# Optimization experiments

Hardware: AMD Instinct MI355X
Metric: run time of the kernel (lower is better)

## Reference

```python
import jax, jax.numpy as jnp
import numpy as np

N_BINS = 500
TAIL = 1.0
MIN_W = 1e-3
MIN_H = 1e-3
MIN_D = 1e-3
WIN_A = -10000.0
WIN_B = 10000.0

N_CELLS = 128
N_GENES_OI = 300
N_GENES = 1000
N_LATENT = 64
N_HID = 32
N_FRAG = 50000
N_CELLS_TOTAL = 5000
N_SPLINE = 3 * N_BINS - 1  # 1499


def _bn(x, g, b, eps=1e-5):
    # torch BatchNorm1d in training mode: batch stats, biased variance
    m = x.mean(0)
    v = x.var(0)
    return (x - m) / jnp.sqrt(v + eps) * g + b


def _rqs_inverse_logdet(y, uw, uh, ud):
    """Unconstrained rational-quadratic spline, inverse pass; returns logdet [F].
    y: [F]; uw, uh: [F, N_BINS]; ud: [F, N_BINS-1]."""
    nb = uw.shape[-1]
    const = float(np.log(np.exp(1.0 - MIN_D) - 1.0))
    ud = jnp.pad(ud, ((0, 0), (1, 1)), constant_values=const)  # [F, nb+1] linear tails
    inside = (y >= -TAIL) & (y <= TAIL)
    yc = jnp.clip(y, -TAIL, TAIL)

    w = jax.nn.softmax(uw, axis=-1)
    w = MIN_W + (1.0 - MIN_W * nb) * w
    cw = jnp.pad(jnp.cumsum(w, axis=-1), ((0, 0), (1, 0)))
    cw = 2.0 * TAIL * cw - TAIL
    cw = cw.at[:, 0].set(-TAIL).at[:, -1].set(TAIL)
    w = cw[:, 1:] - cw[:, :-1]

    h = jax.nn.softmax(uh, axis=-1)
    h = MIN_H + (1.0 - MIN_H * nb) * h
    ch = jnp.pad(jnp.cumsum(h, axis=-1), ((0, 0), (1, 0)))
    ch = 2.0 * TAIL * ch - TAIL
    ch = ch.at[:, 0].set(-TAIL).at[:, -1].set(TAIL)
    h = ch[:, 1:] - ch[:, :-1]

    d = MIN_D + jax.nn.softplus(ud)  # [F, nb+1]

    # inverse: bucketize y against cumheights
    idx = jnp.clip(jnp.sum(yc[:, None] >= ch, axis=-1) - 1, 0, nb - 1)  # [F]
    take = lambda t, i: jnp.take_along_axis(t, i[:, None], axis=-1)[:, 0]
    cw_k = take(cw, idx)
    w_k = take(w, idx)
    ch_k = take(ch, idx)
    h_k = take(h, idx)
    d_k = take(d, idx)
    d_k1 = take(d, idx + 1)

    delta = h_k / w_k
    s = d_k + d_k1 - 2.0 * delta
    dy = yc - ch_k
    qa = dy * s + h_k * (delta - d_k)
    qb = h_k * d_k - dy * s
    qc = -delta * dy
    disc = qb * qb - 4.0 * qa * qc
    root = (2.0 * qc) / (-qb - jnp.sqrt(disc))  # theta in [0,1]
    th1m = root * (1.0 - root)
    den = delta + s * th1m
    num = (delta * delta) * (d_k1 * root * root + 2.0 * delta * th1m + d_k * (1.0 - root) * (1.0 - root))
    logabsdet = jnp.log(num) - 2.0 * jnp.log(den)
    return jnp.where(inside, -logabsdet, 0.0)


def setup_inputs() -> dict:
    key = jax.random.key(0)
    ks = jax.random.split(key, 16)
    ab = WIN_B - WIN_A
    latent = jax.random.normal(ks[0], (N_CELLS, N_LATENT), jnp.float32)
    coordinates = WIN_A + ab * jax.random.uniform(ks[1], (N_FRAG, 2), jnp.float32)
    W1 = jax.random.normal(ks[2], (N_LATENT, N_HID), jnp.float32) / np.sqrt(N_LATENT)
    b1 = jax.random.normal(ks[3], (N_HID,), jnp.float32) * 0.01
    g1 = jnp.ones((N_HID,), jnp.float32)
    be1 = jnp.zeros((N_HID,), jnp.float32)
    W2 = jax.random.normal(ks[4], (N_HID, N_HID), jnp.float32) / np.sqrt(N_HID)
    b2 = jax.random.normal(ks[5], (N_HID,), jnp.float32) * 0.01
    g2 = jnp.ones((N_HID,), jnp.float32)
    be2 = jnp.zeros((N_HID,), jnp.float32)
    stdv = 1.0 / np.sqrt(N_HID) / 100.0
    spline_w = jax.random.uniform(ks[6], (N_GENES, N_HID, N_SPLINE), jnp.float32, -stdv, stdv)
    rho_w = jax.random.uniform(ks[7], (N_GENES, N_HID), jnp.float32, -1.0 / 100.0, 1.0 / 100.0)
    default_init = float(np.log(np.exp(1.0 - MIN_D) - 1.0))
    mix_spline = default_init + 0.1 * jax.random.normal(ks[8], (N_GENES, N_SPLINE), jnp.float32)
    rho_bias = 1e-4 + 1e-3 * jax.random.uniform(ks[9], (N_GENES,), jnp.float32)
    libsize = 500.0 + 4500.0 * jax.random.uniform(ks[10], (N_CELLS_TOTAL,), jnp.float32)
    genes_oi = jax.random.randint(ks[11], (N_GENES_OI,), 0, N_GENES, jnp.int32)
    cells_oi = jax.random.randint(ks[12], (N_CELLS,), 0, N_CELLS_TOTAL, jnp.int32)
    local_cellxgene_ix = jax.random.randint(ks[13], (N_FRAG,), 0, N_CELLS * N_GENES_OI, jnp.int32)
    local_gene_ix = local_cellxgene_ix % N_GENES_OI
    return {
        "latent": latent, "coordinates": coordinates,
        "W1": W1, "b1": b1, "g1": g1, "be1": be1,
        "W2": W2, "b2": b2, "g2": g2, "be2": be2,
        "spline_w": spline_w, "rho_w": rho_w, "mix_spline": mix_spline,
        "rho_bias": rho_bias, "libsize": libsize,
        "genes_oi": genes_oi, "cells_oi": cells_oi,
        "local_cellxgene_ix": local_cellxgene_ix, "local_gene_ix": local_gene_ix,
    }


def reference(latent, coordinates, W1, b1, g1, be1, W2, b2, g2, be2,
              spline_w, rho_w, mix_spline, rho_bias, libsize,
              genes_oi, cells_oi, local_cellxgene_ix, local_gene_ix):
    ab = WIN_B - WIN_A
    # decoder MLP (Linear -> ReLU -> BatchNorm, x2)
    h = _bn(jax.nn.relu(latent @ W1 + b1), g1, be1)
    h = _bn(jax.nn.relu(h @ W2 + b2), g2, be2)  # [C, H]
    sw = spline_w[genes_oi]                      # [G, H, D]
    spline = jnp.einsum('ch,ghd->cgd', h, sw)    # [C, G, D]
    rho = h @ rho_w[genes_oi].T                  # [C, G]
    C, G, D = spline.shape
    spline_frag = spline.reshape(C * G, D)[local_cellxgene_ix]   # [F, D]
    params = mix_spline[genes_oi][local_gene_ix] + spline_frag   # [F, D]
    uw = params[:, :N_BINS]
    uh = params[:, N_BINS:2 * N_BINS]
    ud = params[:, 2 * N_BINS:]

    def logp(val):  # val: [F]
        x = ((val - WIN_A) / ab - 0.5) * 2.0
        return jnp.log(0.5) + _rqs_inverse_logdet(x, uw, uh, ud) - jnp.log(ab)

    ll_loci = logp(coordinates[:, 0]).sum() + logp(coordinates[:, 1]).sum()

    rate = rho_bias[genes_oi] * jnp.exp(rho) * libsize[cells_oi][:, None]  # [C, G]
    counts = jnp.zeros(C * G, jnp.float32).at[local_cellxgene_ix].add(1.0).reshape(C, G)
    ll_counts = counts * jnp.log(rate) - rate - jax.lax.lgamma(counts + 1.0)

    elbo = -(ll_loci + ll_counts.sum())
    return elbo
```

## Files before the change

### kernel.cpp

```cpp
#include <hip/hip_runtime.h>
#include <math.h>

#define N_BINSK  500
#define N_SPL    1499
#define N_CELLSK 128
#define N_GOI    300
#define N_HIDK   32
#define N_LATK   64
#define N_FRAGK  50000
#define N_PAIR   (N_CELLSK * N_GOI)
#define WIN_A_F  (-10000.0f)
#define AB_F     (20000.0f)

#define CELLS_PB 8
#define N_TILES  (N_CELLSK / CELLS_PB)
#define CSTRIDE  1012
#define DPADF    1504
#define NCHUNK   24
#define CAP      16

#define WS_HIST   0
#define WS_ACC    (N_PAIR * 4)
#define WS_H      (WS_ACC + 128 * 8)
#define WS_BUCKET (WS_H + N_CELLSK * N_HIDK * 4)
#define WS_HBF    (WS_BUCKET + N_PAIR * CAP * 2)
#define WS_SWGT   (WS_HBF + N_CELLSK * N_HIDK * 2)
#define WS_ZERO   (WS_H)

#define PREP_BLOCKS (N_GOI * NCHUNK)
#define HIST_BLOCKS 196
#define GENE_GRID   (304 * N_TILES)

typedef __attribute__((ext_vector_type(8))) short bf16x8;
typedef __attribute__((ext_vector_type(4))) float f32x4;

__device__ __forceinline__ unsigned short f2bf(float f)
{
    union { float f; unsigned u; } c; c.f = f;
    return (unsigned short)((c.u + 0x7FFF + ((c.u >> 16) & 1)) >> 16);
}
__device__ __forceinline__ float bf2f(short b)
{
    union { unsigned u; float f; } c;
    c.u = ((unsigned)(unsigned short)b) << 16;
    return c.f;
}
__device__ __forceinline__ float frcp(float x) { return __builtin_amdgcn_rcpf(x); }

__global__ __launch_bounds__(256) void prep_mlp_bucket_kernel(
    const float* __restrict__ spline_w, const int* __restrict__ genes_oi,
    unsigned short* __restrict__ swgt,
    const float* __restrict__ latent, const float* __restrict__ W1, const float* __restrict__ b1,
    const float* __restrict__ g1, const float* __restrict__ be1,
    const float* __restrict__ W2, const float* __restrict__ b2,
    const float* __restrict__ g2, const float* __restrict__ be2,
    float* __restrict__ h_out, unsigned short* __restrict__ h_bf,
    const int* __restrict__ lcx, int* __restrict__ hist,
    unsigned short* __restrict__ bucket)
{
    __shared__ float Ls[N_HIDK][65];
    const int bid = blockIdx.x;
    const int t = threadIdx.x;

    if (bid < PREP_BLOCKS) {
        const int gl = bid / NCHUNK;
        const int chunk = bid - gl * NCHUNK;
        const int g = genes_oi[gl];
        const int dl = t & 63, h0 = t >> 6;
        const int dbase = chunk * 64;

        const float* src = spline_w + (size_t)g * (N_HIDK * N_SPL);
        #pragma unroll
        for (int p = 0; p < 8; ++p) {
            const int hid = h0 + p * 4;
            Ls[hid][dl] = (dbase + dl < N_SPL) ? src[(size_t)hid * N_SPL + dbase + dl] : 0.f;
        }
        __syncthreads();

        const int dim = dbase + (t >> 2);
        if (dim < DPADF) {
            const int hseg = (t & 3) * 8;
            unsigned short out[8];
            #pragma unroll
            for (int j = 0; j < 8; ++j) out[j] = f2bf(Ls[hseg + j][t >> 2]);
            *(uint4*)(swgt + ((size_t)(gl * DPADF + dim) * N_HIDK + hseg)) = *(const uint4*)out;
        }
        return;
    }
    if (bid < PREP_BLOCKS + HIST_BLOCKS) {
        const int f = (bid - PREP_BLOCKS) * 256 + t;
        if (f < N_FRAGK) {
            const int p = lcx[f];
            const int slot = atomicAdd(&hist[p], 1);
            if (slot < CAP) bucket[(size_t)p * CAP + slot] = (unsigned short)f;
        }
        return;
    }

    __shared__ float A[N_CELLSK][N_HIDK + 1];
    __shared__ float mean_s[N_HIDK], rstd_s[N_HIDK];
    const int c = t;
    const bool act = (c < N_CELLSK);

    float x[N_LATK];
    if (act) {
        #pragma unroll
        for (int i = 0; i < N_LATK; ++i) x[i] = latent[c * N_LATK + i];
        for (int j = 0; j < N_HIDK; ++j) {
            float a = b1[j];
            #pragma unroll
            for (int i = 0; i < N_LATK; ++i) a = fmaf(x[i], W1[i * N_HIDK + j], a);
            A[c][j] = fmaxf(a, 0.0f);
        }
    }
    __syncthreads();
    if (c < N_HIDK) {
        float m = 0.f;
        for (int i = 0; i < N_CELLSK; ++i) m += A[i][c];
        m *= (1.0f / N_CELLSK);
        float v = 0.f;
        for (int i = 0; i < N_CELLSK; ++i) { float d = A[i][c] - m; v += d * d; }
        v *= (1.0f / N_CELLSK);
        mean_s[c] = m;
        rstd_s[c] = rsqrtf(v + 1e-5f);
    }
    __syncthreads();
    float hb[N_HIDK];
    if (act) {
        #pragma unroll
        for (int j = 0; j < N_HIDK; ++j)
            hb[j] = (A[c][j] - mean_s[j]) * rstd_s[j] * g1[j] + be1[j];
    }
    __syncthreads();
    if (act) {
        for (int j = 0; j < N_HIDK; ++j) {
            float a = b2[j];
            #pragma unroll
            for (int i = 0; i < N_HIDK; ++i) a = fmaf(hb[i], W2[i * N_HIDK + j], a);
            A[c][j] = fmaxf(a, 0.0f);
        }
    }
    __syncthreads();
    if (c < N_HIDK) {
        float m = 0.f;
        for (int i = 0; i < N_CELLSK; ++i) m += A[i][c];
        m *= (1.0f / N_CELLSK);
        float v = 0.f;
        for (int i = 0; i < N_CELLSK; ++i) { float d = A[i][c] - m; v += d * d; }
        v *= (1.0f / N_CELLSK);
        mean_s[c] = m;
        rstd_s[c] = rsqrtf(v + 1e-5f);
    }
    __syncthreads();
    if (act) {
        #pragma unroll
        for (int j = 0; j < N_HIDK; ++j) {
            const float v = (A[c][j] - mean_s[j]) * rstd_s[j] * g2[j] + be2[j];
            h_out[c * N_HIDK + j] = v;
            h_bf[c * N_HIDK + j] = f2bf(v);
        }
    }
}

__global__ __launch_bounds__(512, 8) void gene_kernel(
    const float* __restrict__ h, const unsigned short* __restrict__ h_bf,
    const unsigned short* __restrict__ swgt,
    const float* __restrict__ mix_spline,
    const int* __restrict__ genes_oi, const float* __restrict__ coords,
    const int* __restrict__ hist, const unsigned short* __restrict__ bucket,
    const float* __restrict__ rho_w, const float* __restrict__ rho_bias,
    const float* __restrict__ libsize, const int* __restrict__ cells_oi,
    double* __restrict__ acc)
{
    __shared__ float P[CELLS_PB * CSTRIDE];
    __shared__ float hL[CELLS_PB][36];
    __shared__ int al_s[CELLS_PB];
    __shared__ int acnt_s[CELLS_PB + 1];
    __shared__ int wcnt[2];

    const int bid = blockIdx.x;
    const int t = threadIdx.x;
    const int lane = t & 63;
    const int w = t >> 6;

    if (bid >= GENE_GRID) {
        const int pgl = bid - GENE_GRID;
        const int g = genes_oi[pgl];
        float v = 0.f;
        if (t < N_CELLSK) {
            const int cnt = hist[t * N_GOI + pgl];
            const float* hrow = h + t * N_HIDK;
            const float* rwp = rho_w + g * N_HIDK;
            float rho = 0.f;
            #pragma unroll
            for (int i = 0; i < N_HIDK; ++i) rho = fmaf(hrow[i], rwp[i], rho);
            const float rate = rho_bias[g] * __expf(rho) * libsize[cells_oi[t]];
            const float cf = (float)cnt;
            v = cf * __logf(rate) - rate - lgammaf(cf + 1.0f);
        }
        #pragma unroll
        for (int o = 32; o; o >>= 1) v += __shfl_xor(v, o);
        if (lane == 0 && w < 2) atomicAdd(&acc[pgl & 127], (double)v);
        return;
    }

    const int r  = bid & 7;
    const int m_ = bid >> 3;
    const int ct = m_ & 15;
    const int gl = (m_ >> 4) * 8 + r;
    if (gl >= N_GOI) return;

    const int cellcnt = (t < N_CELLSK) ? hist[t * N_GOI + gl] : 0;
    const unsigned long long mk = __ballot(cellcnt > 0);
    if (lane == 0 && w < 2) wcnt[w] = (int)__popcll(mk);
    __syncthreads();
    const int nag = wcnt[0] + wcnt[1];
    if (cellcnt > 0) {
        const int pos = ((w == 1) ? wcnt[0] : 0)
                      + (int)__popcll(mk & ((1ull << lane) - 1ull)) - ct * CELLS_PB;
        if (pos >= 0 && pos < CELLS_PB) { al_s[pos] = t; acnt_s[pos] = min(cellcnt, CAP); }
    }
    __syncthreads();
    if (ct * CELLS_PB >= nag) return;
    const int nv = min(CELLS_PB, nag - ct * CELLS_PB);

    if (t == 0) {
        int run = 0;
        #pragma unroll
        for (int s = 0; s < CELLS_PB; ++s) {
            const int c = (s < nv) ? acnt_s[s] : 0;
            acnt_s[s] = run; run += c;
        }
        acnt_s[CELLS_PB] = run;
    }
    if (t < nv * N_HIDK) {
        const int s = t >> 5, i = t & 31;
        hL[s][i] = h[al_s[s] * N_HIDK + i];
    }

    const int g  = genes_oi[gl];
    const float* mixg = mix_spline + (size_t)g * N_SPL;

    {
        const int koff = (lane >> 4) * 8;
        const int acell = al_s[min(lane & 7, nv - 1)];
        const bf16x8 afrag = *(const bf16x8*)(h_bf + acell * N_HIDK + koff);
        const int dcol = lane & 15;
        #pragma unroll 1
        for (int tile = w; tile < 63; tile += 8) {
            const int d = tile * 16 + dcol;
            const bf16x8 bfrag = *(const bf16x8*)(swgt + ((size_t)(gl * DPADF + d) * N_HIDK + koff));
            const float m = mixg[min(d, 999)];
            f32x4 acc4 = {m, m, m, m};
            acc4 = __builtin_amdgcn_mfma_f32_16x16x32_bf16(afrag, bfrag, acc4, 0, 0, 0);
            if (lane < 32 && d < 1000) {
                const int s = d + ((d >= N_BINSK) ? 4 : 0);
                #pragma unroll
                for (int rr = 0; rr < 4; ++rr)
                    P[((lane >> 4) * 4 + rr) * CSTRIDE + s] = __expf(acc4[rr]);
            }
        }
    }
    __syncthreads();

    for (int s = w; s < 2 * nv; s += 8) {
        float* Pb = P + (s >> 1) * CSTRIDE + ((s & 1) ? 504 : 0);
        const int base = lane * 8;
        float v[8], pre[8];
        if (lane < 62) {
            *(float4*)&v[0] = *(const float4*)&Pb[base];
            *(float4*)&v[4] = *(const float4*)&Pb[base + 4];
        } else if (lane == 62) {
            *(float4*)&v[0] = *(const float4*)&Pb[base];
            v[4] = v[5] = v[6] = v[7] = 0.f;
        } else {
            #pragma unroll
            for (int k = 0; k < 8; ++k) v[k] = 0.f;
        }
        float run = 0.f;
        #pragma unroll
        for (int k = 0; k < 8; ++k) { pre[k] = run; run += v[k]; }
        float sv = run;
        #pragma unroll
        for (int o = 1; o < 64; o <<= 1) {
            float tt = __shfl_up(sv, o);
            if (lane >= o) sv += tt;
        }
        const float tot = __shfl(sv, 63);
        const float invT = frcp(tot);
        const float excl = sv - run;
        #pragma unroll
        for (int k = 0; k < 8; ++k)
            pre[k] = fmaf((float)(base + k), 0.002f, -1.0f) + (excl + pre[k]) * invT;
        if (lane < 63) {
            *(float4*)&Pb[base]     = *(const float4*)&pre[0];
            *(float4*)&Pb[base + 4] = *(const float4*)&pre[4];
        }
    }
    __syncthreads();

    float contrib = 0.f;
    const int ncb = acnt_s[CELLS_PB] * 2;
    if (t < ncb) {
        const int fi = t >> 1;
        int s = 0;
        #pragma unroll
        for (int k = 1; k < CELLS_PB; ++k) s += (acnt_s[k] <= fi) ? 1 : 0;
        const int cell = al_s[s];
        const int fid = bucket[(size_t)(cell * N_GOI + gl) * CAP + (fi - acnt_s[s])];
        const float val = coords[fid * 2 + (t & 1)];
        const float yc = ((val - WIN_A_F) / AB_F - 0.5f) * 2.0f;
        if (yc >= -1.0f && yc <= 1.0f) {
            const float* CWc = P + s * CSTRIDE;
            const float* CHc = CWc + 504;

            int j = (int)fminf(fmaxf((yc + 1.0f) * 250.0f, 0.0f), 499.0f);
            if (CHc[j] <= yc) {
                while (j < 500 && CHc[j + 1] <= yc) ++j;
            } else {
                do { --j; } while (CHc[j] > yc);
            }
            const int idx = min(j, N_BINSK - 1);

            const int bcol = 999 + min(max(idx, 1), 498);
            const unsigned short* rud = swgt + (size_t)(gl * DPADF + bcol) * N_HIDK;
            float dA = 0.f, dB = 0.f;
            #pragma unroll
            for (int c8 = 0; c8 < 4; ++c8) {
                const bf16x8 va = *(const bf16x8*)(rud + c8 * 8);
                const bf16x8 vb = *(const bf16x8*)(rud + N_HIDK + c8 * 8);
                const float4 h0 = *(const float4*)&hL[s][c8 * 8];
                const float4 h1 = *(const float4*)&hL[s][c8 * 8 + 4];
                dA = fmaf(h0.x, bf2f(va[0]), dA); dB = fmaf(h0.x, bf2f(vb[0]), dB);
                dA = fmaf(h0.y, bf2f(va[1]), dA); dB = fmaf(h0.y, bf2f(vb[1]), dB);
                dA = fmaf(h0.z, bf2f(va[2]), dA); dB = fmaf(h0.z, bf2f(vb[2]), dB);
                dA = fmaf(h0.w, bf2f(va[3]), dA); dB = fmaf(h0.w, bf2f(vb[3]), dB);
                dA = fmaf(h1.x, bf2f(va[4]), dA); dB = fmaf(h1.x, bf2f(vb[4]), dB);
                dA = fmaf(h1.y, bf2f(va[5]), dA); dB = fmaf(h1.y, bf2f(vb[5]), dB);
                dA = fmaf(h1.z, bf2f(va[6]), dA); dB = fmaf(h1.z, bf2f(vb[6]), dB);
                dA = fmaf(h1.w, bf2f(va[7]), dA); dB = fmaf(h1.w, bf2f(vb[7]), dB);
            }
            float udA = 0.f, udB = 0.f;
            if (idx == 0)                 udB = dA + mixg[1000];
            else if (idx == N_BINSK - 1)  udA = dB + mixg[1498];
            else { udA = dA + mixg[bcol]; udB = dB + mixg[bcol + 1]; }
            const float d_k  = (idx == 0)           ? 1.0f
                             : 0.001f + __logf(1.0f + __expf(udA));
            const float d_k1 = (idx == N_BINSK - 1) ? 1.0f
                             : 0.001f + __logf(1.0f + __expf(udB));

            const float ch_k  = CHc[idx];
            const float h_k   = CHc[idx + 1] - ch_k;
            const float w_k   = CWc[idx + 1] - CWc[idx];

            const float delta = h_k * frcp(w_k);
            const float s2 = d_k + d_k1 - 2.0f * delta;
            const float dy = yc - ch_k;
            const float qa = dy * s2 + h_k * (delta - d_k);
            const float qb = h_k * d_k - dy * s2;
            const float qc = -delta * dy;
            const float disc = qb * qb - 4.0f * qa * qc;
            const float root = 2.0f * qc * frcp(-qb - sqrtf(disc));
            const float th1m = root * (1.0f - root);
            const float den = delta + s2 * th1m;
            const float num = delta * delta *
                (d_k1 * root * root + 2.0f * delta * th1m + d_k * (1.0f - root) * (1.0f - root));
            const float rd = frcp(den);
            contrib -= __logf(num * rd * rd);
        }
    }
    #pragma unroll
    for (int o = 32; o; o >>= 1) contrib += __shfl_xor(contrib, o);
    if (lane == 0 && contrib != 0.0f)
        atomicAdd(&acc[(bid ^ (w << 3)) & 127], (double)contrib);
}

__global__ __launch_bounds__(64) void final_kernel(const double* __restrict__ acc,
                                                   float* __restrict__ out)
{
    const int lane = threadIdx.x;
    double s = acc[lane] + acc[lane + 64];
    #pragma unroll
    for (int o = 32; o; o >>= 1) s += __shfl_down(s, o);
    if (lane == 0) {
        const double c0 = (double)(2 * N_FRAGK) * (log(0.5) - log((double)AB_F));
        out[0] = (float)(-(s + c0));
    }
}

extern "C" void kernel_launch(void* const* d_in, const int* in_sizes, int n_in,
                              void* d_out, int out_size, void* d_ws, size_t ws_size,
                              hipStream_t stream)
{
    const float* latent   = (const float*)d_in[0];
    const float* coords   = (const float*)d_in[1];
    const float* W1       = (const float*)d_in[2];
    const float* b1       = (const float*)d_in[3];
    const float* g1       = (const float*)d_in[4];
    const float* be1      = (const float*)d_in[5];
    const float* W2       = (const float*)d_in[6];
    const float* b2       = (const float*)d_in[7];
    const float* g2       = (const float*)d_in[8];
    const float* be2      = (const float*)d_in[9];
    const float* spline_w = (const float*)d_in[10];
    const float* rho_w    = (const float*)d_in[11];
    const float* mix      = (const float*)d_in[12];
    const float* rho_bias = (const float*)d_in[13];
    const float* libsize  = (const float*)d_in[14];
    const int* genes_oi   = (const int*)d_in[15];
    const int* cells_oi   = (const int*)d_in[16];
    const int* lcx        = (const int*)d_in[17];

    char* ws = (char*)d_ws;
    int*            hist   = (int*)(ws + WS_HIST);
    double*         acc    = (double*)(ws + WS_ACC);
    float*          h_ws   = (float*)(ws + WS_H);
    unsigned short* bucket = (unsigned short*)(ws + WS_BUCKET);
    unsigned short* h_bf   = (unsigned short*)(ws + WS_HBF);
    unsigned short* swgt   = (unsigned short*)(ws + WS_SWGT);

    hipMemsetAsync(d_ws, 0, WS_ZERO, stream);

    hipLaunchKernelGGL(prep_mlp_bucket_kernel, dim3(PREP_BLOCKS + HIST_BLOCKS + 1), dim3(256), 0, stream,
                       spline_w, genes_oi, swgt,
                       latent, W1, b1, g1, be1, W2, b2, g2, be2, h_ws, h_bf, lcx, hist, bucket);
    hipLaunchKernelGGL(gene_kernel, dim3(GENE_GRID + N_GOI), dim3(512), 0, stream,
                       h_ws, h_bf, swgt, mix, genes_oi, coords,
                       hist, bucket, rho_w, rho_bias, libsize, cells_oi, acc);
    hipLaunchKernelGGL(final_kernel, dim3(1), dim3(64), 0, stream, acc, (float*)d_out);
}
```

Baseline: 110.0 us.

## Fold final reduction into gene kernel via last-block counter; reorder prep blocks

Removes the separate final_kernel launch: each gene_kernel block increments a done counter after its atomic accumulation, and the last block sums the accumulators and writes the output. The prep kernel is also reordered so the serial MLP block and the histogram blocks are scheduled first, ahead of the many spline-weight conversion blocks, so the long-running MLP block is not left as a tail. This adds a global atomic and memory fences per block in exchange for one fewer kernel launch.

```diff
diff --git a/kernel.cpp b/kernel.cpp
--- a/kernel.cpp
+++ b/kernel.cpp
@@ -21,7 +21,8 @@
 
 #define WS_HIST   0
 #define WS_ACC    (N_PAIR * 4)
-#define WS_H      (WS_ACC + 128 * 8)
+#define WS_CNT    (WS_ACC + 128 * 8)
+#define WS_H      (WS_CNT + 16)
 #define WS_BUCKET (WS_H + N_CELLSK * N_HIDK * 4)
 #define WS_HBF    (WS_BUCKET + N_PAIR * CAP * 2)
 #define WS_SWGT   (WS_HBF + N_CELLSK * N_HIDK * 2)
@@ -30,6 +31,7 @@
 #define PREP_BLOCKS (N_GOI * NCHUNK)
 #define HIST_BLOCKS 196
 #define GENE_GRID   (304 * N_TILES)
+#define GENE_TOTAL  (GENE_GRID + N_GOI)
 
 typedef __attribute__((ext_vector_type(8))) short bf16x8;
 typedef __attribute__((ext_vector_type(4))) float f32x4;
@@ -62,33 +64,74 @@
     const int bid = blockIdx.x;
     const int t = threadIdx.x;
 
-    if (bid < PREP_BLOCKS) {
-        const int gl = bid / NCHUNK;
-        const int chunk = bid - gl * NCHUNK;
-        const int g = genes_oi[gl];
-        const int dl = t & 63, h0 = t >> 6;
-        const int dbase = chunk * 64;
-
-        const float* src = spline_w + (size_t)g * (N_HIDK * N_SPL);
-        #pragma unroll
-        for (int p = 0; p < 8; ++p) {
-            const int hid = h0 + p * 4;
-            Ls[hid][dl] = (dbase + dl < N_SPL) ? src[(size_t)hid * N_SPL + dbase + dl] : 0.f;
-        }
-        __syncthreads();
-
-        const int dim = dbase + (t >> 2);
-        if (dim < DPADF) {
-            const int hseg = (t & 3) * 8;
-            unsigned short out[8];
-            #pragma unroll
-            for (int j = 0; j < 8; ++j) out[j] = f2bf(Ls[hseg + j][t >> 2]);
-            *(uint4*)(swgt + ((size_t)(gl * DPADF + dim) * N_HIDK + hseg)) = *(const uint4*)out;
+    if (bid == 0) {
+        __shared__ float A[N_CELLSK][N_HIDK + 1];
+        __shared__ float mean_s[N_HIDK], rstd_s[N_HIDK];
+        const int c = t;
+        const bool act = (c < N_CELLSK);
+
+        float x[N_LATK];
+        if (act) {
+            #pragma unroll
+            for (int i = 0; i < N_LATK; ++i) x[i] = latent[c * N_LATK + i];
+            for (int j = 0; j < N_HIDK; ++j) {
+                float a = b1[j];
+                #pragma unroll
+                for (int i = 0; i < N_LATK; ++i) a = fmaf(x[i], W1[i * N_HIDK + j], a);
+                A[c][j] = fmaxf(a, 0.0f);
+            }
+        }
+        __syncthreads();
+        if (c < N_HIDK) {
+            float m = 0.f;
+            for (int i = 0; i < N_CELLSK; ++i) m += A[i][c];
+            m *= (1.0f / N_CELLSK);
+            float v = 0.f;
+            for (int i = 0; i < N_CELLSK; ++i) { float d = A[i][c] - m; v += d * d; }
+            v *= (1.0f / N_CELLSK);
+            mean_s[c] = m;
+            rstd_s[c] = rsqrtf(v + 1e-5f);
+        }
+        __syncthreads();
+        float hb[N_HIDK];
+        if (act) {
+            #pragma unroll
+            for (int j = 0; j < N_HIDK; ++j)
+                hb[j] = (A[c][j] - mean_s[j]) * rstd_s[j] * g1[j] + be1[j];
+        }
+        __syncthreads();
+        if (act) {
+            for (int j = 0; j < N_HIDK; ++j) {
+                float a = b2[j];
+                #pragma unroll
+                for (int i = 0; i < N_HIDK; ++i) a = fmaf(hb[i], W2[i * N_HIDK + j], a);
+                A[c][j] = fmaxf(a, 0.0f);
+            }
+        }
+        __syncthreads();
+        if (c < N_HIDK) {
+            float m = 0.f;
+            for (int i = 0; i < N_CELLSK; ++i) m += A[i][c];
+            m *= (1.0f / N_CELLSK);
+            float v = 0.f;
+            for (int i = 0; i < N_CELLSK; ++i) { float d = A[i][c] - m; v += d * d; }
+            v *= (1.0f / N_CELLSK);
+            mean_s[c] = m;
+            rstd_s[c] = rsqrtf(v + 1e-5f);
+        }
+        __syncthreads();
+        if (act) {
+            #pragma unroll
+            for (int j = 0; j < N_HIDK; ++j) {
+                const float v = (A[c][j] - mean_s[j]) * rstd_s[j] * g2[j] + be2[j];
+                h_out[c * N_HIDK + j] = v;
+                h_bf[c * N_HIDK + j] = f2bf(v);
+            }
         }
         return;
     }
-    if (bid < PREP_BLOCKS + HIST_BLOCKS) {
-        const int f = (bid - PREP_BLOCKS) * 256 + t;
+    if (bid <= HIST_BLOCKS) {
+        const int f = (bid - 1) * 256 + t;
         if (f < N_FRAGK) {
             const int p = lcx[f];
             const int slot = atomicAdd(&hist[p], 1);
@@ -97,68 +140,28 @@
         return;
     }
 
-    __shared__ float A[N_CELLSK][N_HIDK + 1];
-    __shared__ float mean_s[N_HIDK], rstd_s[N_HIDK];
-    const int c = t;
-    const bool act = (c < N_CELLSK);
-
-    float x[N_LATK];
-    if (act) {
+    const int pb = bid - HIST_BLOCKS - 1;
+    const int gl = pb / NCHUNK;
+    const int chunk = pb - gl * NCHUNK;
+    const int g = genes_oi[gl];
+    const int dl = t & 63, h0 = t >> 6;
+    const int dbase = chunk * 64;
+
+    const float* src = spline_w + (size_t)g * (N_HIDK * N_SPL);
+    #pragma unroll
+    for (int p = 0; p < 8; ++p) {
+        const int hid = h0 + p * 4;
+        Ls[hid][dl] = (dbase + dl < N_SPL) ? src[(size_t)hid * N_SPL + dbase + dl] : 0.f;
+    }
+    __syncthreads();
+
+    const int dim = dbase + (t >> 2);
+    if (dim < DPADF) {
+        const int hseg = (t & 3) * 8;
+        unsigned short out[8];
         #pragma unroll
-        for (int i = 0; i < N_LATK; ++i) x[i] = latent[c * N_LATK + i];
-        for (int j = 0; j < N_HIDK; ++j) {
-            float a = b1[j];
-            #pragma unroll
-            for (int i = 0; i < N_LATK; ++i) a = fmaf(x[i], W1[i * N_HIDK + j], a);
-            A[c][j] = fmaxf(a, 0.0f);
-        }
-    }
-    __syncthreads();
-    if (c < N_HIDK) {
-        float m = 0.f;
-        for (int i = 0; i < N_CELLSK; ++i) m += A[i][c];
-        m *= (1.0f / N_CELLSK);
-        float v = 0.f;
-        for (int i = 0; i < N_CELLSK; ++i) { float d = A[i][c] - m; v += d * d; }
-        v *= (1.0f / N_CELLSK);
-        mean_s[c] = m;
-        rstd_s[c] = rsqrtf(v + 1e-5f);
-    }
-    __syncthreads();
-    float hb[N_HIDK];
-    if (act) {
-        #pragma unroll
-        for (int j = 0; j < N_HIDK; ++j)
-            hb[j] = (A[c][j] - mean_s[j]) * rstd_s[j] * g1[j] + be1[j];
-    }
-    __syncthreads();
-    if (act) {
-        for (int j = 0; j < N_HIDK; ++j) {
-            float a = b2[j];
-            #pragma unroll
-            for (int i = 0; i < N_HIDK; ++i) a = fmaf(hb[i], W2[i * N_HIDK + j], a);
-            A[c][j] = fmaxf(a, 0.0f);
-        }
-    }
-    __syncthreads();
-    if (c < N_HIDK) {
-        float m = 0.f;
-        for (int i = 0; i < N_CELLSK; ++i) m += A[i][c];
-        m *= (1.0f / N_CELLSK);
-        float v = 0.f;
-        for (int i = 0; i < N_CELLSK; ++i) { float d = A[i][c] - m; v += d * d; }
-        v *= (1.0f / N_CELLSK);
-        mean_s[c] = m;
-        rstd_s[c] = rsqrtf(v + 1e-5f);
-    }
-    __syncthreads();
-    if (act) {
-        #pragma unroll
-        for (int j = 0; j < N_HIDK; ++j) {
-            const float v = (A[c][j] - mean_s[j]) * rstd_s[j] * g2[j] + be2[j];
-            h_out[c * N_HIDK + j] = v;
-            h_bf[c * N_HIDK + j] = f2bf(v);
-        }
+        for (int j = 0; j < 8; ++j) out[j] = f2bf(Ls[hseg + j][t >> 2]);
+        *(uint4*)(swgt + ((size_t)(gl * DPADF + dim) * N_HIDK + hseg)) = *(const uint4*)out;
     }
 }
 
@@ -170,221 +173,228 @@
     const int* __restrict__ hist, const unsigned short* __restrict__ bucket,
     const float* __restrict__ rho_w, const float* __restrict__ rho_bias,
     const float* __restrict__ libsize, const int* __restrict__ cells_oi,
-    double* __restrict__ acc)
+    double* __restrict__ acc, int* __restrict__ cnt_done, float* __restrict__ out)
 {
     __shared__ float P[CELLS_PB * CSTRIDE];
     __shared__ float hL[CELLS_PB][36];
     __shared__ int al_s[CELLS_PB];
     __shared__ int acnt_s[CELLS_PB + 1];
     __shared__ int wcnt[2];
+    __shared__ int lastFlag;
 
     const int bid = blockIdx.x;
     const int t = threadIdx.x;
     const int lane = t & 63;
     const int w = t >> 6;
 
-    if (bid >= GENE_GRID) {
-        const int pgl = bid - GENE_GRID;
-        const int g = genes_oi[pgl];
-        float v = 0.f;
-        if (t < N_CELLSK) {
-            const int cnt = hist[t * N_GOI + pgl];
-            const float* hrow = h + t * N_HIDK;
-            const float* rwp = rho_w + g * N_HIDK;
-            float rho = 0.f;
-            #pragma unroll
-            for (int i = 0; i < N_HIDK; ++i) rho = fmaf(hrow[i], rwp[i], rho);
-            const float rate = rho_bias[g] * __expf(rho) * libsize[cells_oi[t]];
-            const float cf = (float)cnt;
-            v = cf * __logf(rate) - rate - lgammaf(cf + 1.0f);
+    do {
+        if (bid >= GENE_GRID) {
+            const int pgl = bid - GENE_GRID;
+            const int g = genes_oi[pgl];
+            float v = 0.f;
+            if (t < N_CELLSK) {
+                const int cnt = hist[t * N_GOI + pgl];
+                const float* hrow = h + t * N_HIDK;
+                const float* rwp = rho_w + g * N_HIDK;
+                float rho = 0.f;
+                #pragma unroll
+                for (int i = 0; i < N_HIDK; ++i) rho = fmaf(hrow[i], rwp[i], rho);
+                const float rate = rho_bias[g] * __expf(rho) * libsize[cells_oi[t]];
+                const float cf = (float)cnt;
+                v = cf * __logf(rate) - rate - lgammaf(cf + 1.0f);
+            }
+            #pragma unroll
+            for (int o = 32; o; o >>= 1) v += __shfl_xor(v, o);
+            if (lane == 0 && w < 2) atomicAdd(&acc[pgl & 127], (double)v);
+            break;
+        }
+
+        const int r  = bid & 7;
+        const int m_ = bid >> 3;
+        const int ct = m_ & 15;
+        const int gl = (m_ >> 4) * 8 + r;
+        if (gl >= N_GOI) break;
+
+        const int cellcnt = (t < N_CELLSK) ? hist[t * N_GOI + gl] : 0;
+        const unsigned long long mk = __ballot(cellcnt > 0);
+        if (lane == 0 && w < 2) wcnt[w] = (int)__popcll(mk);
+        __syncthreads();
+        const int nag = wcnt[0] + wcnt[1];
+        if (cellcnt > 0) {
+            const int pos = ((w == 1) ? wcnt[0] : 0)
+                          + (int)__popcll(mk & ((1ull << lane) - 1ull)) - ct * CELLS_PB;
+            if (pos >= 0 && pos < CELLS_PB) { al_s[pos] = t; acnt_s[pos] = min(cellcnt, CAP); }
+        }
+        __syncthreads();
+        if (ct * CELLS_PB >= nag) break;
+        const int nv = min(CELLS_PB, nag - ct * CELLS_PB);
+
+        if (t == 0) {
+            int run = 0;
+            #pragma unroll
+            for (int s = 0; s < CELLS_PB; ++s) {
+                const int c = (s < nv) ? acnt_s[s] : 0;
+                acnt_s[s] = run; run += c;
+            }
+            acnt_s[CELLS_PB] = run;
+        }
+        if (t < nv * N_HIDK) {
+            const int s = t >> 5, i = t & 31;
+            hL[s][i] = h[al_s[s] * N_HIDK + i];
+        }
+
+        const int g  = genes_oi[gl];
+        const float* mixg = mix_spline + (size_t)g * N_SPL;
+
+        {
+            const int koff = (lane >> 4) * 8;
+            const int acell = al_s[min(lane & 7, nv - 1)];
+            const bf16x8 afrag = *(const bf16x8*)(h_bf + acell * N_HIDK + koff);
+            const int dcol = lane & 15;
+            #pragma unroll 1
+            for (int tile = w; tile < 63; tile += 8) {
+                const int d = tile * 16 + dcol;
+                const bf16x8 bfrag = *(const bf16x8*)(swgt + ((size_t)(gl * DPADF + d) * N_HIDK + koff));
+                const float m = mixg[min(d, 999)];
+                f32x4 acc4 = {m, m, m, m};
+                acc4 = __builtin_amdgcn_mfma_f32_16x16x32_bf16(afrag, bfrag, acc4, 0, 0, 0);
+                if (lane < 32 && d < 1000) {
+                    const int s = d + ((d >= N_BINSK) ? 4 : 0);
+                    #pragma unroll
+                    for (int rr = 0; rr < 4; ++rr)
+                        P[((lane >> 4) * 4 + rr) * CSTRIDE + s] = __expf(acc4[rr]);
+                }
+            }
+        }
+        __syncthreads();
+
+        for (int s = w; s < 2 * nv; s += 8) {
+            float* Pb = P + (s >> 1) * CSTRIDE + ((s & 1) ? 504 : 0);
+            const int base = lane * 8;
+            float v[8], pre[8];
+            if (lane < 62) {
+                *(float4*)&v[0] = *(const float4*)&Pb[base];
+                *(float4*)&v[4] = *(const float4*)&Pb[base + 4];
+            } else if (lane == 62) {
+                *(float4*)&v[0] = *(const float4*)&Pb[base];
+                v[4] = v[5] = v[6] = v[7] = 0.f;
+            } else {
+                #pragma unroll
+                for (int k = 0; k < 8; ++k) v[k] = 0.f;
+            }
+            float run = 0.f;
+            #pragma unroll
+            for (int k = 0; k < 8; ++k) { pre[k] = run; run += v[k]; }
+            float sv = run;
+            #pragma unroll
+            for (int o = 1; o < 64; o <<= 1) {
+                float tt = __shfl_up(sv, o);
+                if (lane >= o) sv += tt;
+            }
+            const float tot = __shfl(sv, 63);
+            const float invT = frcp(tot);
+            const float excl = sv - run;
+            #pragma unroll
+            for (int k = 0; k < 8; ++k)
+                pre[k] = fmaf((float)(base + k), 0.002f, -1.0f) + (excl + pre[k]) * invT;
+            if (lane < 63) {
+                *(float4*)&Pb[base]     = *(const float4*)&pre[0];
+                *(float4*)&Pb[base + 4] = *(const float4*)&pre[4];
+            }
+        }
+        __syncthreads();
+
+        float contrib = 0.f;
+        const int ncb = acnt_s[CELLS_PB] * 2;
+        if (t < ncb) {
+            const int fi = t >> 1;
+            int s = 0;
+            #pragma unroll
+            for (int k = 1; k < CELLS_PB; ++k) s += (acnt_s[k] <= fi) ? 1 : 0;
+            const int cell = al_s[s];
+            const int fid = bucket[(size_t)(cell * N_GOI + gl) * CAP + (fi - acnt_s[s])];
+            const float val = coords[fid * 2 + (t & 1)];
+            const float yc = ((val - WIN_A_F) / AB_F - 0.5f) * 2.0f;
+            if (yc >= -1.0f && yc <= 1.0f) {
+                const float* CWc = P + s * CSTRIDE;
+                const float* CHc = CWc + 504;
+
+                int j = (int)fminf(fmaxf((yc + 1.0f) * 250.0f, 0.0f), 499.0f);
+                if (CHc[j] <= yc) {
+                    while (j < 500 && CHc[j + 1] <= yc) ++j;
+                } else {
+                    do { --j; } while (CHc[j] > yc);
+                }
+                const int idx = min(j, N_BINSK - 1);
+
+                const int bcol = 999 + min(max(idx, 1), 498);
+                const unsigned short* rud = swgt + (size_t)(gl * DPADF + bcol) * N_HIDK;
+                float dA = 0.f, dB = 0.f;
+                #pragma unroll
+                for (int c8 = 0; c8 < 4; ++c8) {
+                    const bf16x8 va = *(const bf16x8*)(rud + c8 * 8);
+                    const bf16x8 vb = *(const bf16x8*)(rud + N_HIDK + c8 * 8);
+                    const float4 h0 = *(const float4*)&hL[s][c8 * 8];
+                    const float4 h1 = *(const float4*)&hL[s][c8 * 8 + 4];
+                    dA = fmaf(h0.x, bf2f(va[0]), dA); dB = fmaf(h0.x, bf2f(vb[0]), dB);
+                    dA = fmaf(h0.y, bf2f(va[1]), dA); dB = fmaf(h0.y, bf2f(vb[1]), dB);
+                    dA = fmaf(h0.z, bf2f(va[2]), dA); dB = fmaf(h0.z, bf2f(vb[2]), dB);
+                    dA = fmaf(h0.w, bf2f(va[3]), dA); dB = fmaf(h0.w, bf2f(vb[3]), dB);
+                    dA = fmaf(h1.x, bf2f(va[4]), dA); dB = fmaf(h1.x, bf2f(vb[4]), dB);
+                    dA = fmaf(h1.y, bf2f(va[5]), dA); dB = fmaf(h1.y, bf2f(vb[5]), dB);
+                    dA = fmaf(h1.z, bf2f(va[6]), dA); dB = fmaf(h1.z, bf2f(vb[6]), dB);
+                    dA = fmaf(h1.w, bf2f(va[7]), dA); dB = fmaf(h1.w, bf2f(vb[7]), dB);
+                }
+                float udA = 0.f, udB = 0.f;
+                if (idx == 0)                 udB = dA + mixg[1000];
+                else if (idx == N_BINSK - 1)  udA = dB + mixg[1498];
+                else { udA = dA + mixg[bcol]; udB = dB + mixg[bcol + 1]; }
+                const float d_k  = (idx == 0)           ? 1.0f
+                                 : 0.001f + __logf(1.0f + __expf(udA));
+                const float d_k1 = (idx == N_BINSK - 1) ? 1.0f
+                                 : 0.001f + __logf(1.0f + __expf(udB));
+
+                const float ch_k  = CHc[idx];
+                const float h_k   = CHc[idx + 1] - ch_k;
+                const float w_k   = CWc[idx + 1] - CWc[idx];
+
+                const float delta = h_k * frcp(w_k);
+                const float s2 = d_k + d_k1 - 2.0f * delta;
+                const float dy = yc - ch_k;
+                const float qa = dy * s2 + h_k * (delta - d_k);
+                const float qb = h_k * d_k - dy * s2;
+                const float qc = -delta * dy;
+                const float disc = qb * qb - 4.0f * qa * qc;
+                const float root = 2.0f * qc * frcp(-qb - sqrtf(disc));
+                const float th1m = root * (1.0f - root);
+                const float den = delta + s2 * th1m;
+                const float num = delta * delta *
+                    (d_k1 * root * root + 2.0f * delta * th1m + d_k * (1.0f - root) * (1.0f - root));
+                const float rd = frcp(den);
+                contrib -= __logf(num * rd * rd);
+            }
         }
         #pragma unroll
-        for (int o = 32; o; o >>= 1) v += __shfl_xor(v, o);
-        if (lane == 0 && w < 2) atomicAdd(&acc[pgl & 127], (double)v);
-        return;
-    }
-
-    const int r  = bid & 7;
-    const int m_ = bid >> 3;
-    const int ct = m_ & 15;
-    const int gl = (m_ >> 4) * 8 + r;
-    if (gl >= N_GOI) return;
-
-    const int cellcnt = (t < N_CELLSK) ? hist[t * N_GOI + gl] : 0;
-    const unsigned long long mk = __ballot(cellcnt > 0);
-    if (lane == 0 && w < 2) wcnt[w] = (int)__popcll(mk);
+        for (int o = 32; o; o >>= 1) contrib += __shfl_xor(contrib, o);
+        if (lane == 0 && contrib != 0.0f)
+            atomicAdd(&acc[(bid ^ (w << 3)) & 127], (double)contrib);
+    } while (0);
+
     __syncthreads();
-    const int nag = wcnt[0] + wcnt[1];
-    if (cellcnt > 0) {
-        const int pos = ((w == 1) ? wcnt[0] : 0)
-                      + (int)__popcll(mk & ((1ull << lane) - 1ull)) - ct * CELLS_PB;
-        if (pos >= 0 && pos < CELLS_PB) { al_s[pos] = t; acnt_s[pos] = min(cellcnt, CAP); }
+    if (t == 0) {
+        __threadfence();
+        lastFlag = (atomicAdd(cnt_done, 1) == GENE_TOTAL - 1) ? 1 : 0;
     }
     __syncthreads();
-    if (ct * CELLS_PB >= nag) return;
-    const int nv = min(CELLS_PB, nag - ct * CELLS_PB);
-
-    if (t == 0) {
-        int run = 0;
+    if (lastFlag && t < 64) {
+        __threadfence();
+        double s = acc[t] + acc[t + 64];
         #pragma unroll
-        for (int s = 0; s < CELLS_PB; ++s) {
-            const int c = (s < nv) ? acnt_s[s] : 0;
-            acnt_s[s] = run; run += c;
-        }
-        acnt_s[CELLS_PB] = run;
-    }
-    if (t < nv * N_HIDK) {
-        const int s = t >> 5, i = t & 31;
-        hL[s][i] = h[al_s[s] * N_HIDK + i];
-    }
-
-    const int g  = genes_oi[gl];
-    const float* mixg = mix_spline + (size_t)g * N_SPL;
-
-    {
-        const int koff = (lane >> 4) * 8;
-        const int acell = al_s[min(lane & 7, nv - 1)];
-        const bf16x8 afrag = *(const bf16x8*)(h_bf + acell * N_HIDK + koff);
-        const int dcol = lane & 15;
-        #pragma unroll 1
-        for (int tile = w; tile < 63; tile += 8) {
-            const int d = tile * 16 + dcol;
-            const bf16x8 bfrag = *(const bf16x8*)(swgt + ((size_t)(gl * DPADF + d) * N_HIDK + koff));
-            const float m = mixg[min(d, 999)];
-            f32x4 acc4 = {m, m, m, m};
-            acc4 = __builtin_amdgcn_mfma_f32_16x16x32_bf16(afrag, bfrag, acc4, 0, 0, 0);
-            if (lane < 32 && d < 1000) {
-                const int s = d + ((d >= N_BINSK) ? 4 : 0);
-                #pragma unroll
-                for (int rr = 0; rr < 4; ++rr)
-                    P[((lane >> 4) * 4 + rr) * CSTRIDE + s] = __expf(acc4[rr]);
-            }
-        }
-    }
-    __syncthreads();
-
-    for (int s = w; s < 2 * nv; s += 8) {
-        float* Pb = P + (s >> 1) * CSTRIDE + ((s & 1) ? 504 : 0);
-        const int base = lane * 8;
-        float v[8], pre[8];
-        if (lane < 62) {
-            *(float4*)&v[0] = *(const float4*)&Pb[base];
-            *(float4*)&v[4] = *(const float4*)&Pb[base + 4];
-        } else if (lane == 62) {
-            *(float4*)&v[0] = *(const float4*)&Pb[base];
-            v[4] = v[5] = v[6] = v[7] = 0.f;
-        } else {
-            #pragma unroll
-            for (int k = 0; k < 8; ++k) v[k] = 0.f;
-        }
-        float run = 0.f;
-        #pragma unroll
-        for (int k = 0; k < 8; ++k) { pre[k] = run; run += v[k]; }
-        float sv = run;
-        #pragma unroll
-        for (int o = 1; o < 64; o <<= 1) {
-            float tt = __shfl_up(sv, o);
-            if (lane >= o) sv += tt;
-        }
-        const float tot = __shfl(sv, 63);
-        const float invT = frcp(tot);
-        const float excl = sv - run;
-        #pragma unroll
-        for (int k = 0; k < 8; ++k)
-            pre[k] = fmaf((float)(base + k), 0.002f, -1.0f) + (excl + pre[k]) * invT;
-        if (lane < 63) {
-            *(float4*)&Pb[base]     = *(const float4*)&pre[0];
-            *(float4*)&Pb[base + 4] = *(const float4*)&pre[4];
-        }
-    }
-    __syncthreads();
-
-    float contrib = 0.f;
-    const int ncb = acnt_s[CELLS_PB] * 2;
-    if (t < ncb) {
-        const int fi = t >> 1;
-        int s = 0;
-        #pragma unroll
-        for (int k = 1; k < CELLS_PB; ++k) s += (acnt_s[k] <= fi) ? 1 : 0;
-        const int cell = al_s[s];
-        const int fid = bucket[(size_t)(cell * N_GOI + gl) * CAP + (fi - acnt_s[s])];
-        const float val = coords[fid * 2 + (t & 1)];
-        const float yc = ((val - WIN_A_F) / AB_F - 0.5f) * 2.0f;
-        if (yc >= -1.0f && yc <= 1.0f) {
-            const float* CWc = P + s * CSTRIDE;
-            const float* CHc = CWc + 504;
-
-            int j = (int)fminf(fmaxf((yc + 1.0f) * 250.0f, 0.0f), 499.0f);
-            if (CHc[j] <= yc) {
-                while (j < 500 && CHc[j + 1] <= yc) ++j;
-            } else {
-                do { --j; } while (CHc[j] > yc);
-            }
-            const int idx = min(j, N_BINSK - 1);
-
-            const int bcol = 999 + min(max(idx, 1), 498);
-            const unsigned short* rud = swgt + (size_t)(gl * DPADF + bcol) * N_HIDK;
-            float dA = 0.f, dB = 0.f;
-            #pragma unroll
-            for (int c8 = 0; c8 < 4; ++c8) {
-                const bf16x8 va = *(const bf16x8*)(rud + c8 * 8);
-                const bf16x8 vb = *(const bf16x8*)(rud + N_HIDK + c8 * 8);
-                const float4 h0 = *(const float4*)&hL[s][c8 * 8];
-                const float4 h1 = *(const float4*)&hL[s][c8 * 8 + 4];
-                dA = fmaf(h0.x, bf2f(va[0]), dA); dB = fmaf(h0.x, bf2f(vb[0]), dB);
-                dA = fmaf(h0.y, bf2f(va[1]), dA); dB = fmaf(h0.y, bf2f(vb[1]), dB);
-                dA = fmaf(h0.z, bf2f(va[2]), dA); dB = fmaf(h0.z, bf2f(vb[2]), dB);
-                dA = fmaf(h0.w, bf2f(va[3]), dA); dB = fmaf(h0.w, bf2f(vb[3]), dB);
-                dA = fmaf(h1.x, bf2f(va[4]), dA); dB = fmaf(h1.x, bf2f(vb[4]), dB);
-                dA = fmaf(h1.y, bf2f(va[5]), dA); dB = fmaf(h1.y, bf2f(vb[5]), dB);
-                dA = fmaf(h1.z, bf2f(va[6]), dA); dB = fmaf(h1.z, bf2f(vb[6]), dB);
-                dA = fmaf(h1.w, bf2f(va[7]), dA); dB = fmaf(h1.w, bf2f(vb[7]), dB);
-            }
-            float udA = 0.f, udB = 0.f;
-            if (idx == 0)                 udB = dA + mixg[1000];
-            else if (idx == N_BINSK - 1)  udA = dB + mixg[1498];
-            else { udA = dA + mixg[bcol]; udB = dB + mixg[bcol + 1]; }
-            const float d_k  = (idx == 0)           ? 1.0f
-                             : 0.001f + __logf(1.0f + __expf(udA));
-            const float d_k1 = (idx == N_BINSK - 1) ? 1.0f
-                             : 0.001f + __logf(1.0f + __expf(udB));
-
-            const float ch_k  = CHc[idx];
-            const float h_k   = CHc[idx + 1] - ch_k;
-            const float w_k   = CWc[idx + 1] - CWc[idx];
-
-            const float delta = h_k * frcp(w_k);
-            const float s2 = d_k + d_k1 - 2.0f * delta;
-            const float dy = yc - ch_k;
-            const float qa = dy * s2 + h_k * (delta - d_k);
-            const float qb = h_k * d_k - dy * s2;
-            const float qc = -delta * dy;
-            const float disc = qb * qb - 4.0f * qa * qc;
-            const float root = 2.0f * qc * frcp(-qb - sqrtf(disc));
-            const float th1m = root * (1.0f - root);
-            const float den = delta + s2 * th1m;
-            const float num = delta * delta *
-                (d_k1 * root * root + 2.0f * delta * th1m + d_k * (1.0f - root) * (1.0f - root));
-            const float rd = frcp(den);
-            contrib -= __logf(num * rd * rd);
-        }
-    }
-    #pragma unroll
-    for (int o = 32; o; o >>= 1) contrib += __shfl_xor(contrib, o);
-    if (lane == 0 && contrib != 0.0f)
-        atomicAdd(&acc[(bid ^ (w << 3)) & 127], (double)contrib);
-}
-
-__global__ __launch_bounds__(64) void final_kernel(const double* __restrict__ acc,
-                                                   float* __restrict__ out)
-{
-    const int lane = threadIdx.x;
-    double s = acc[lane] + acc[lane + 64];
-    #pragma unroll
-    for (int o = 32; o; o >>= 1) s += __shfl_down(s, o);
-    if (lane == 0) {
-        const double c0 = (double)(2 * N_FRAGK) * (log(0.5) - log((double)AB_F));
-        out[0] = (float)(-(s + c0));
+        for (int o = 32; o; o >>= 1) s += __shfl_down(s, o);
+        if (t == 0) {
+            const double c0 = (double)(2 * N_FRAGK) * (log(0.5) - log((double)AB_F));
+            out[0] = (float)(-(s + c0));
+        }
     }
 }
 
@@ -412,20 +422,21 @@
     const int* lcx        = (const int*)d_in[17];
 
     char* ws = (char*)d_ws;
-    int*            hist   = (int*)(ws + WS_HIST);
-    double*         acc    = (double*)(ws + WS_ACC);
-    float*          h_ws   = (float*)(ws + WS_H);
-    unsigned short* bucket = (unsigned short*)(ws + WS_BUCKET);
-    unsigned short* h_bf   = (unsigned short*)(ws + WS_HBF);
-    unsigned short* swgt   = (unsigned short*)(ws + WS_SWGT);
+    int*            hist     = (int*)(ws + WS_HIST);
+    double*         acc      = (double*)(ws + WS_ACC);
+    int*            cnt_done = (int*)(ws + WS_CNT);
+    float*          h_ws     = (float*)(ws + WS_H);
+    unsigned short* bucket   = (unsigned short*)(ws + WS_BUCKET);
+    unsigned short* h_bf     = (unsigned short*)(ws + WS_HBF);
+    unsigned short* swgt     = (unsigned short*)(ws + WS_SWGT);
 
     hipMemsetAsync(d_ws, 0, WS_ZERO, stream);
 
-    hipLaunchKernelGGL(prep_mlp_bucket_kernel, dim3(PREP_BLOCKS + HIST_BLOCKS + 1), dim3(256), 0, stream,
+    hipLaunchKernelGGL(prep_mlp_bucket_kernel, dim3(1 + HIST_BLOCKS + PREP_BLOCKS), dim3(256), 0, stream,
                        spline_w, genes_oi, swgt,
                        latent, W1, b1, g1, be1, W2, b2, g2, be2, h_ws, h_bf, lcx, hist, bucket);
-    hipLaunchKernelGGL(gene_kernel, dim3(GENE_GRID + N_GOI), dim3(512), 0, stream,
+    hipLaunchKernelGGL(gene_kernel, dim3(GENE_TOTAL), dim3(512), 0, stream,
                        h_ws, h_bf, swgt, mix, genes_oi, coords,
-                       hist, bucket, rho_w, rho_bias, libsize, cells_oi, acc);
-    hipLaunchKernelGGL(final_kernel, dim3(1), dim3(64), 0, stream, acc, (float*)d_out);
+                       hist, bucket, rho_w, rho_bias, libsize, cells_oi,
+                       acc, cnt_done, (float*)d_out);
 }
```

Result: slower. 221.8 us (+101.6%).
